# Optimization experiments

Hardware: AMD Instinct MI355X
Metric: run time of the kernel (lower is better)

## Reference

```python
import jax, jax.numpy as jnp
import numpy as np

N_NODES = 50000


def setup_inputs() -> dict:
    key = jax.random.key(0)
    k1, k2, k3, k4, k5, k6 = jax.random.split(key, 6)
    N, E, D, F = 50000, 800000, 512, 256
    feature_ori = jax.random.normal(k1, (N, D), dtype=jnp.float32)
    feature_aug = jax.random.normal(k2, (N, D), dtype=jnp.float32)
    edge_row = jax.random.randint(k3, (E,), 0, N, dtype=jnp.int32)
    edge_col = jax.random.randint(k4, (E,), 0, N, dtype=jnp.int32)
    edge_val = jax.random.uniform(k5, (E,), dtype=jnp.float32)
    # kaiming-uniform-ish init for weight, zeros for bias (as in reset_parameters)
    bound = float(np.sqrt(6.0 / D))
    weight = jax.random.uniform(k6, (D, F), dtype=jnp.float32, minval=-bound, maxval=bound)
    bias = jnp.zeros((F,), dtype=jnp.float32)
    return {
        "feature_ori": feature_ori,
        "feature_aug": feature_aug,
        "edge_row": edge_row,
        "edge_col": edge_col,
        "edge_val": edge_val,
        "weight": weight,
        "bias": bias,
    }


def _branch(feat, weight, bias, edge_row, edge_col, edge_val):
    # support = X @ W  -> [N, F]
    support = feat @ weight
    # sparse aggregation: out[i] = sum_{e: row[e]=i} val[e] * support[col[e]]
    msgs = edge_val[:, None] * support[edge_col]          # [E, F]
    out = jax.ops.segment_sum(msgs, edge_row, num_segments=N_NODES)
    return jax.nn.relu(out + bias)


def reference(feature_ori, feature_aug, edge_row, edge_col, edge_val, weight, bias):
    out_ori = _branch(feature_ori, weight, bias, edge_row, edge_col, edge_val)
    out_aug = _branch(feature_aug, weight, bias, edge_row, edge_col, edge_val)
    return (out_ori, out_aug)
```

## Files before the change

### kernel.cpp

```cpp
#include <hip/hip_runtime.h>
#include <hip/hip_bf16.h>

#define NNODES 50000
#define NEDGES 800000
#define DIN    512
#define FOUT   256

typedef __attribute__((ext_vector_type(8))) short short8;
typedef __attribute__((ext_vector_type(4))) float f32x4;
typedef __attribute__((ext_vector_type(4))) unsigned int u32x4;
typedef __attribute__((ext_vector_type(4))) unsigned short usv4;
typedef __attribute__((ext_vector_type(8))) unsigned short usv8;

static __device__ __forceinline__ unsigned short f2bf(float f) {
    unsigned int u = __float_as_uint(f);
    u += 0x7FFF + ((u >> 16) & 1);
    return (unsigned short)(u >> 16);
}
static __device__ __forceinline__ float bf2f(unsigned short h) {
    return __uint_as_float(((unsigned int)h) << 16);
}

__global__ void prep_kernel(const float* __restrict__ W, unsigned short* __restrict__ Wt,
                            const int* __restrict__ row, int* __restrict__ cnt) {
    int b = blockIdx.x;
    if (b < 512) {
        int o = b * 256 + threadIdx.x;
        int n = o >> 9, k = o & 511;
        Wt[o] = f2bf(W[k * FOUT + n]);
    } else {
        int e = (b - 512) * 256 + threadIdx.x;
        if (e < NEDGES) atomicAdd(&cnt[row[e]], 1);
    }
}

__global__ void scan_partial(const int* __restrict__ cnt, int* __restrict__ partial) {
    __shared__ int sm[256];
    int i = blockIdx.x * 256 + threadIdx.x;
    int v = (i < NNODES) ? cnt[i] : 0;
    sm[threadIdx.x] = v; __syncthreads();
    for (int s = 128; s > 0; s >>= 1) {
        if (threadIdx.x < s) sm[threadIdx.x] += sm[threadIdx.x + s];
        __syncthreads();
    }
    if (threadIdx.x == 0) partial[blockIdx.x] = sm[0];
}

__global__ void scan_exclusive_small(int* __restrict__ partial, int nb) {
    __shared__ int sm[256];
    int t = threadIdx.x;
    int v = (t < nb) ? partial[t] : 0;
    sm[t] = v; __syncthreads();
    for (int off = 1; off < 256; off <<= 1) {
        int add = (t >= off) ? sm[t - off] : 0;
        __syncthreads();
        sm[t] += add;
        __syncthreads();
    }
    if (t < nb) partial[t] = sm[t] - v;
}

__global__ void scan_write(const int* __restrict__ cnt, const int* __restrict__ partial,
                           int* __restrict__ row_start, int* __restrict__ cursor) {
    __shared__ int sm[256];
    int t = threadIdx.x;
    int i = blockIdx.x * 256 + t;
    int v = (i < NNODES) ? cnt[i] : 0;
    sm[t] = v; __syncthreads();
    for (int off = 1; off < 256; off <<= 1) {
        int add = (t >= off) ? sm[t - off] : 0;
        __syncthreads();
        sm[t] += add;
        __syncthreads();
    }
    if (i < NNODES) {
        int rs = partial[blockIdx.x] + sm[t] - v;
        row_start[i] = rs;
        cursor[i] = rs;
    }
    if (i == 0) row_start[NNODES] = NEDGES;
}

__global__ void scatter_kernel(const int* __restrict__ row, const int* __restrict__ col,
                               const float* __restrict__ val,
                               int* __restrict__ cursor, unsigned int* __restrict__ cv) {
    int e = blockIdx.x * 256 + threadIdx.x;
    if (e < NEDGES) {
        int r = row[e];
        int pos = atomicAdd(&cursor[r], 1);
        unsigned int vb = f2bf(val[e]);
        cv[pos] = (vb << 16) | (unsigned int)col[e];
    }
}

__global__ __launch_bounds__(512, 2)
void gemm_kernel(const float* __restrict__ Xo, const float* __restrict__ Xa,
                 const unsigned short* __restrict__ Wt,
                 unsigned short* __restrict__ S) {
    __shared__ __align__(16) unsigned short As[2][128][40];
    __shared__ __align__(16) unsigned short Bs[2][256][40];
    const int tid = threadIdx.x;
    const int branch = blockIdx.z;
    const float* __restrict__ X = branch ? Xa : Xo;
    const int boff = branch * 256;
    const int m_base = blockIdx.x * 128;
    const int lane = tid & 63, wave = tid >> 6;
    const int wm = (wave >> 2) * 64, wn = (wave & 3) * 64;
    const int quad = lane >> 4, r16 = lane & 15;

    f32x4 acc[4][4] = {};

    const int colf  = (tid & 7) * 4;
    const int rbase = tid >> 3;
    const int kseg  = (tid & 3) * 8;
    const int nrow  = tid >> 2;

    const int gm0 = m_base + rbase;
    const int gm1 = m_base + 64 + rbase;
    const bool va0 = gm0 < NNODES, va1 = gm1 < NNODES;
    const float* pA0 = &X[(long)gm0 * DIN + colf];
    const float* pA1 = &X[(long)gm1 * DIN + colf];
    const unsigned short* pB0 = &Wt[(long)nrow * DIN + kseg];
    const unsigned short* pB1 = &Wt[(long)(128 + nrow) * DIN + kseg];

    f32x4 fa0, fa1; u32x4 ub0, ub1;

#define GEMM_LOAD(K0)                                                          \
    do {                                                                       \
        fa0 = va0 ? __builtin_nontemporal_load((const f32x4*)(pA0 + (K0)))     \
                  : (f32x4)0.f;                                                \
        fa1 = va1 ? __builtin_nontemporal_load((const f32x4*)(pA1 + (K0)))     \
                  : (f32x4)0.f;                                                \
        ub0 = *(const u32x4*)(pB0 + (K0));                                     \
        ub1 = *(const u32x4*)(pB1 + (K0));                                     \
    } while (0)

#define GEMM_WRITE(B)                                                          \
    do {                                                                       \
        usv4 h0; h0.x = f2bf(fa0[0]); h0.y = f2bf(fa0[1]);                     \
        h0.z = f2bf(fa0[2]); h0.w = f2bf(fa0[3]);                              \
        *(usv4*)&As[B][rbase][colf] = h0;                                      \
        usv4 h1; h1.x = f2bf(fa1[0]); h1.y = f2bf(fa1[1]);                     \
        h1.z = f2bf(fa1[2]); h1.w = f2bf(fa1[3]);                              \
        *(usv4*)&As[B][64 + rbase][colf] = h1;                                 \
        *(u32x4*)&Bs[B][nrow][kseg] = ub0;                                     \
        *(u32x4*)&Bs[B][128 + nrow][kseg] = ub1;                               \
    } while (0)

#define GEMM_COMPUTE(B)                                                        \
    do {                                                                       \
        short8 a_frag[4], b_frag[4];                                           \
        _Pragma("unroll")                                                      \
        for (int mi = 0; mi < 4; mi++)                                         \
            a_frag[mi] = *(const short8*)&As[B][wm + mi * 16 + r16][quad * 8]; \
        _Pragma("unroll")                                                      \
        for (int ni = 0; ni < 4; ni++)                                         \
            b_frag[ni] = *(const short8*)&Bs[B][wn + ni * 16 + r16][quad * 8]; \
        _Pragma("unroll")                                                      \
        for (int mi = 0; mi < 4; mi++)                                         \
            _Pragma("unroll")                                                  \
            for (int ni = 0; ni < 4; ni++)                                     \
                acc[mi][ni] = __builtin_amdgcn_mfma_f32_16x16x32_bf16(         \
                    a_frag[mi], b_frag[ni], acc[mi][ni], 0, 0, 0);             \
    } while (0)

    GEMM_LOAD(0);
    GEMM_WRITE(0);
    __syncthreads();

    for (int k0 = 0; k0 < DIN; k0 += 64) {
        GEMM_LOAD(k0 + 32);
        GEMM_COMPUTE(0);
        GEMM_WRITE(1);
        __syncthreads();
        if (k0 + 64 < DIN) GEMM_LOAD(k0 + 64);
        GEMM_COMPUTE(1);
        if (k0 + 64 < DIN) GEMM_WRITE(0);
        __syncthreads();
    }

#undef GEMM_LOAD
#undef GEMM_WRITE
#undef GEMM_COMPUTE

    #pragma unroll
    for (int mi = 0; mi < 4; mi++) {
        #pragma unroll
        for (int rr = 0; rr < 4; rr++) {
            int m = m_base + wm + mi * 16 + quad * 4 + rr;
            if (m < NNODES) {
                #pragma unroll
                for (int ni = 0; ni < 4; ni++) {
                    int n = wn + ni * 16 + r16;
                    S[(long)m * 512 + boff + n] = f2bf(acc[mi][ni][rr]);
                }
            }
        }
    }
}

__global__ __launch_bounds__(256)
void aggregate_kernel(const int* __restrict__ row_start,
                      const unsigned int* __restrict__ cv,
                      const unsigned short* __restrict__ S,
                      const float* __restrict__ bias, float* __restrict__ out) {
    int node = blockIdx.x * 4 + (threadIdx.x >> 6);
    int lane = threadIdx.x & 63;
    if (node >= NNODES) return;
    int s = row_start[node], e = row_start[node + 1];
    const int f8 = (lane & 31) * 8;
    const long soff = (long)(lane >> 5) * 256 + f8;
    float a0 = 0.f, a1 = 0.f, a2 = 0.f, a3 = 0.f;
    float a4 = 0.f, a5 = 0.f, a6 = 0.f, a7 = 0.f;

#define LOADG(C0, C1, C2, C3, Q0, Q1, Q2, Q3, I)                               \
    do {                                                                       \
        C0 = __builtin_nontemporal_load(&cv[(I)]);                             \
        C1 = __builtin_nontemporal_load(&cv[(I) + 1]);                         \
        C2 = __builtin_nontemporal_load(&cv[(I) + 2]);                         \
        C3 = __builtin_nontemporal_load(&cv[(I) + 3]);                         \
        Q0 = *(const usv8*)&S[(long)(C0 & 0xFFFFu) * 512 + soff];              \
        Q1 = *(const usv8*)&S[(long)(C1 & 0xFFFFu) * 512 + soff];              \
        Q2 = *(const usv8*)&S[(long)(C2 & 0xFFFFu) * 512 + soff];              \
        Q3 = *(const usv8*)&S[(long)(C3 & 0xFFFFu) * 512 + soff];              \
    } while (0)

#define EDGE_FMA(Cw, Q)                                                        \
    do {                                                                       \
        float v = bf2f((unsigned short)((Cw) >> 16));                          \
        a0 = fmaf(v, bf2f((Q)[0]), a0); a1 = fmaf(v, bf2f((Q)[1]), a1);        \
        a2 = fmaf(v, bf2f((Q)[2]), a2); a3 = fmaf(v, bf2f((Q)[3]), a3);        \
        a4 = fmaf(v, bf2f((Q)[4]), a4); a5 = fmaf(v, bf2f((Q)[5]), a5);        \
        a6 = fmaf(v, bf2f((Q)[6]), a6); a7 = fmaf(v, bf2f((Q)[7]), a7);        \
    } while (0)

#define FMAG(C0, C1, C2, C3, Q0, Q1, Q2, Q3)                                   \
    do {                                                                       \
        EDGE_FMA(C0, Q0); EDGE_FMA(C1, Q1);                                    \
        EDGE_FMA(C2, Q2); EDGE_FMA(C3, Q3);                                    \
    } while (0)

    unsigned int c0, c1, c2, c3, d0, d1, d2, d3;
    usv8 qa0, qa1, qa2, qa3, qb0, qb1, qb2, qb3;

    int idx = s;
    int r = (e - s) >> 2;
    if (r > 0) {
        LOADG(c0, c1, c2, c3, qa0, qa1, qa2, qa3, idx); idx += 4; r--;
        while (r >= 2) {
            LOADG(d0, d1, d2, d3, qb0, qb1, qb2, qb3, idx); idx += 4;
            FMAG(c0, c1, c2, c3, qa0, qa1, qa2, qa3);
            LOADG(c0, c1, c2, c3, qa0, qa1, qa2, qa3, idx); idx += 4;
            FMAG(d0, d1, d2, d3, qb0, qb1, qb2, qb3);
            r -= 2;
        }
        if (r == 1) {
            LOADG(d0, d1, d2, d3, qb0, qb1, qb2, qb3, idx); idx += 4;
            FMAG(c0, c1, c2, c3, qa0, qa1, qa2, qa3);
            FMAG(d0, d1, d2, d3, qb0, qb1, qb2, qb3);
        } else {
            FMAG(c0, c1, c2, c3, qa0, qa1, qa2, qa3);
        }
    }
    for (; idx < e; idx++) {
        unsigned int w = __builtin_nontemporal_load(&cv[idx]);
        usv8 q = *(const usv8*)&S[(long)(w & 0xFFFFu) * 512 + soff];
        EDGE_FMA(w, q);
    }

#undef LOADG
#undef EDGE_FMA
#undef FMAG

    f32x4 b0 = *(const f32x4*)&bias[f8];
    f32x4 b1 = *(const f32x4*)&bias[f8 + 4];
    long o = (long)(lane >> 5) * NNODES * FOUT + (long)node * FOUT + f8;
    f32x4 r0, r1;
    r0[0] = fmaxf(a0 + b0[0], 0.f); r0[1] = fmaxf(a1 + b0[1], 0.f);
    r0[2] = fmaxf(a2 + b0[2], 0.f); r0[3] = fmaxf(a3 + b0[3], 0.f);
    r1[0] = fmaxf(a4 + b1[0], 0.f); r1[1] = fmaxf(a5 + b1[1], 0.f);
    r1[2] = fmaxf(a6 + b1[2], 0.f); r1[3] = fmaxf(a7 + b1[3], 0.f);
    __builtin_nontemporal_store(r0, (f32x4*)&out[o]);
    __builtin_nontemporal_store(r1, (f32x4*)&out[o + 4]);
}

extern "C" void kernel_launch(void* const* d_in, const int* in_sizes, int n_in,
                              void* d_out, int out_size, void* d_ws, size_t ws_size,
                              hipStream_t stream) {
    const float* Xo   = (const float*)d_in[0];
    const float* Xa   = (const float*)d_in[1];
    const int*   erow = (const int*)d_in[2];
    const int*   ecol = (const int*)d_in[3];
    const float* eval_= (const float*)d_in[4];
    const float* W    = (const float*)d_in[5];
    const float* bias = (const float*)d_in[6];
    float* out = (float*)d_out;

    char* ws = (char*)d_ws;
    unsigned short* S         = (unsigned short*)(ws);
    unsigned short* Wt        = (unsigned short*)(ws + 51200000);
    int*            cnt       = (int*)(ws + 51462144);
    int*            row_start = (int*)(ws + 51662144);
    int*            partial   = (int*)(ws + 51862208);
    unsigned int*   cv        = (unsigned int*)(ws + 51863232);

    (void)in_sizes; (void)n_in; (void)out_size; (void)ws_size;

    hipMemsetAsync(cnt, 0, 200000, stream);
    prep_kernel<<<3637, 256, 0, stream>>>(W, Wt, erow, cnt);
    scan_partial<<<196, 256, 0, stream>>>(cnt, partial);
    scan_exclusive_small<<<1, 256, 0, stream>>>(partial, 196);
    scan_write<<<196, 256, 0, stream>>>(cnt, partial, row_start, cnt);
    scatter_kernel<<<3125, 256, 0, stream>>>(erow, ecol, eval_, cnt, cv);

    dim3 gg(391, 1, 2);
    gemm_kernel<<<gg, 512, 0, stream>>>(Xo, Xa, Wt, S);

    aggregate_kernel<<<12500, 256, 0, stream>>>(row_start, cv, S, bias, out);
}
```

Before: 487.0 us.

## Split aggregation into per-branch passes with half-wave edge parallelism

Aggregation now runs as two launches, one per branch (ori/aug). Within each pass the two half-waves take alternate edges of the same node, then combine partial sums with a cross-lane shuffle before writing. The aim is to shrink the working set of gathered S rows per pass so it fits better in cache and improves gather locality. In exchange it adds a second launch, reads the edge list twice, and adds shuffle-reduction overhead.

```diff
diff --git a/kernel.cpp b/kernel.cpp
--- a/kernel.cpp
+++ b/kernel.cpp
@@ -200,88 +200,113 @@
 }
 
 __global__ __launch_bounds__(256)
-void aggregate_kernel(const int* __restrict__ row_start,
-                      const unsigned int* __restrict__ cv,
-                      const unsigned short* __restrict__ S,
-                      const float* __restrict__ bias, float* __restrict__ out) {
-    int node = blockIdx.x * 4 + (threadIdx.x >> 6);
-    int lane = threadIdx.x & 63;
+void aggregate_pass(const int* __restrict__ row_start,
+                    const unsigned int* __restrict__ cv,
+                    const unsigned short* __restrict__ S,
+                    const float* __restrict__ bias, float* __restrict__ out,
+                    const int half) {
+    const int node = __builtin_amdgcn_readfirstlane(blockIdx.x * 4 + (threadIdx.x >> 6));
     if (node >= NNODES) return;
-    int s = row_start[node], e = row_start[node + 1];
-    const int f8 = (lane & 31) * 8;
-    const long soff = (long)(lane >> 5) * 256 + f8;
+    const int lane = threadIdx.x & 63;
+    const int fl = (lane & 31) * 8;
+    const unsigned int sub = lane >> 5;
+    const long soff = (long)half * 256 + fl;
+    const int s = row_start[node], e = row_start[node + 1];
+
     float a0 = 0.f, a1 = 0.f, a2 = 0.f, a3 = 0.f;
     float a4 = 0.f, a5 = 0.f, a6 = 0.f, a7 = 0.f;
 
-#define LOADG(C0, C1, C2, C3, Q0, Q1, Q2, Q3, I)                               \
-    do {                                                                       \
-        C0 = __builtin_nontemporal_load(&cv[(I)]);                             \
-        C1 = __builtin_nontemporal_load(&cv[(I) + 1]);                         \
-        C2 = __builtin_nontemporal_load(&cv[(I) + 2]);                         \
-        C3 = __builtin_nontemporal_load(&cv[(I) + 3]);                         \
-        Q0 = *(const usv8*)&S[(long)(C0 & 0xFFFFu) * 512 + soff];              \
-        Q1 = *(const usv8*)&S[(long)(C1 & 0xFFFFu) * 512 + soff];              \
-        Q2 = *(const usv8*)&S[(long)(C2 & 0xFFFFu) * 512 + soff];              \
-        Q3 = *(const usv8*)&S[(long)(C3 & 0xFFFFu) * 512 + soff];              \
-    } while (0)
-
-#define EDGE_FMA(Cw, Q)                                                        \
-    do {                                                                       \
-        float v = bf2f((unsigned short)((Cw) >> 16));                          \
+#define PLOAD(CW0, CW1, Q)                                                     \
+    do {                                                                       \
+        unsigned int cw_ = sub ? (CW1) : (CW0);                                \
+        Q = *(const usv8*)&S[(long)(cw_ & 0xFFFFu) * 512 + soff];              \
+    } while (0)
+
+#define PFMA(CW0, CW1, Q)                                                      \
+    do {                                                                       \
+        unsigned int cw_ = sub ? (CW1) : (CW0);                                \
+        float v = bf2f((unsigned short)(cw_ >> 16));                           \
         a0 = fmaf(v, bf2f((Q)[0]), a0); a1 = fmaf(v, bf2f((Q)[1]), a1);        \
         a2 = fmaf(v, bf2f((Q)[2]), a2); a3 = fmaf(v, bf2f((Q)[3]), a3);        \
         a4 = fmaf(v, bf2f((Q)[4]), a4); a5 = fmaf(v, bf2f((Q)[5]), a5);        \
         a6 = fmaf(v, bf2f((Q)[6]), a6); a7 = fmaf(v, bf2f((Q)[7]), a7);        \
     } while (0)
 
-#define FMAG(C0, C1, C2, C3, Q0, Q1, Q2, Q3)                                   \
-    do {                                                                       \
-        EDGE_FMA(C0, Q0); EDGE_FMA(C1, Q1);                                    \
-        EDGE_FMA(C2, Q2); EDGE_FMA(C3, Q3);                                    \
-    } while (0)
-
-    unsigned int c0, c1, c2, c3, d0, d1, d2, d3;
+#define LOADG(C0, C1, C2, C3, C4, C5, C6, C7, Q0, Q1, Q2, Q3, I)               \
+    do {                                                                       \
+        C0 = cv[(I)];     C1 = cv[(I) + 1]; C2 = cv[(I) + 2]; C3 = cv[(I) + 3];\
+        C4 = cv[(I) + 4]; C5 = cv[(I) + 5]; C6 = cv[(I) + 6]; C7 = cv[(I) + 7];\
+        PLOAD(C0, C1, Q0); PLOAD(C2, C3, Q1);                                  \
+        PLOAD(C4, C5, Q2); PLOAD(C6, C7, Q3);                                  \
+    } while (0)
+
+#define FMAG(C0, C1, C2, C3, C4, C5, C6, C7, Q0, Q1, Q2, Q3)                   \
+    do {                                                                       \
+        PFMA(C0, C1, Q0); PFMA(C2, C3, Q1);                                    \
+        PFMA(C4, C5, Q2); PFMA(C6, C7, Q3);                                    \
+    } while (0)
+
+    unsigned int c0, c1, c2, c3, c4, c5, c6, c7;
+    unsigned int d0, d1, d2, d3, d4, d5, d6, d7;
     usv8 qa0, qa1, qa2, qa3, qb0, qb1, qb2, qb3;
 
     int idx = s;
-    int r = (e - s) >> 2;
+    int r = (e - s) >> 3;
     if (r > 0) {
-        LOADG(c0, c1, c2, c3, qa0, qa1, qa2, qa3, idx); idx += 4; r--;
+        LOADG(c0, c1, c2, c3, c4, c5, c6, c7, qa0, qa1, qa2, qa3, idx); idx += 8; r--;
         while (r >= 2) {
-            LOADG(d0, d1, d2, d3, qb0, qb1, qb2, qb3, idx); idx += 4;
-            FMAG(c0, c1, c2, c3, qa0, qa1, qa2, qa3);
-            LOADG(c0, c1, c2, c3, qa0, qa1, qa2, qa3, idx); idx += 4;
-            FMAG(d0, d1, d2, d3, qb0, qb1, qb2, qb3);
+            LOADG(d0, d1, d2, d3, d4, d5, d6, d7, qb0, qb1, qb2, qb3, idx); idx += 8;
+            FMAG(c0, c1, c2, c3, c4, c5, c6, c7, qa0, qa1, qa2, qa3);
+            LOADG(c0, c1, c2, c3, c4, c5, c6, c7, qa0, qa1, qa2, qa3, idx); idx += 8;
+            FMAG(d0, d1, d2, d3, d4, d5, d6, d7, qb0, qb1, qb2, qb3);
             r -= 2;
         }
         if (r == 1) {
-            LOADG(d0, d1, d2, d3, qb0, qb1, qb2, qb3, idx); idx += 4;
-            FMAG(c0, c1, c2, c3, qa0, qa1, qa2, qa3);
-            FMAG(d0, d1, d2, d3, qb0, qb1, qb2, qb3);
+            LOADG(d0, d1, d2, d3, d4, d5, d6, d7, qb0, qb1, qb2, qb3, idx); idx += 8;
+            FMAG(c0, c1, c2, c3, c4, c5, c6, c7, qa0, qa1, qa2, qa3);
+            FMAG(d0, d1, d2, d3, d4, d5, d6, d7, qb0, qb1, qb2, qb3);
         } else {
-            FMAG(c0, c1, c2, c3, qa0, qa1, qa2, qa3);
+            FMAG(c0, c1, c2, c3, c4, c5, c6, c7, qa0, qa1, qa2, qa3);
         }
     }
-    for (; idx < e; idx++) {
-        unsigned int w = __builtin_nontemporal_load(&cv[idx]);
+    for (; idx + 2 <= e; idx += 2) {
+        unsigned int w0 = cv[idx], w1 = cv[idx + 1];
+        usv8 q;
+        PLOAD(w0, w1, q);
+        PFMA(w0, w1, q);
+    }
+    if (idx < e) {
+        unsigned int w = cv[idx];
         usv8 q = *(const usv8*)&S[(long)(w & 0xFFFFu) * 512 + soff];
-        EDGE_FMA(w, q);
-    }
-
+        float v = sub ? 0.f : bf2f((unsigned short)(w >> 16));
+        a0 = fmaf(v, bf2f(q[0]), a0); a1 = fmaf(v, bf2f(q[1]), a1);
+        a2 = fmaf(v, bf2f(q[2]), a2); a3 = fmaf(v, bf2f(q[3]), a3);
+        a4 = fmaf(v, bf2f(q[4]), a4); a5 = fmaf(v, bf2f(q[5]), a5);
+        a6 = fmaf(v, bf2f(q[6]), a6); a7 = fmaf(v, bf2f(q[7]), a7);
+    }
+
+#undef PLOAD
+#undef PFMA
 #undef LOADG
-#undef EDGE_FMA
 #undef FMAG
 
-    f32x4 b0 = *(const f32x4*)&bias[f8];
-    f32x4 b1 = *(const f32x4*)&bias[f8 + 4];
-    long o = (long)(lane >> 5) * NNODES * FOUT + (long)node * FOUT + f8;
-    f32x4 r0, r1;
-    r0[0] = fmaxf(a0 + b0[0], 0.f); r0[1] = fmaxf(a1 + b0[1], 0.f);
-    r0[2] = fmaxf(a2 + b0[2], 0.f); r0[3] = fmaxf(a3 + b0[3], 0.f);
-    r1[0] = fmaxf(a4 + b1[0], 0.f); r1[1] = fmaxf(a5 + b1[1], 0.f);
-    r1[2] = fmaxf(a6 + b1[2], 0.f); r1[3] = fmaxf(a7 + b1[3], 0.f);
-    __builtin_nontemporal_store(r0, (f32x4*)&out[o]);
-    __builtin_nontemporal_store(r1, (f32x4*)&out[o + 4]);
+    a0 += __shfl_xor(a0, 32); a1 += __shfl_xor(a1, 32);
+    a2 += __shfl_xor(a2, 32); a3 += __shfl_xor(a3, 32);
+    a4 += __shfl_xor(a4, 32); a5 += __shfl_xor(a5, 32);
+    a6 += __shfl_xor(a6, 32); a7 += __shfl_xor(a7, 32);
+
+    if (lane < 32) {
+        f32x4 b0 = *(const f32x4*)&bias[fl];
+        f32x4 b1 = *(const f32x4*)&bias[fl + 4];
+        long o = (long)half * NNODES * FOUT + (long)node * FOUT + fl;
+        f32x4 r0, r1;
+        r0[0] = fmaxf(a0 + b0[0], 0.f); r0[1] = fmaxf(a1 + b0[1], 0.f);
+        r0[2] = fmaxf(a2 + b0[2], 0.f); r0[3] = fmaxf(a3 + b0[3], 0.f);
+        r1[0] = fmaxf(a4 + b1[0], 0.f); r1[1] = fmaxf(a5 + b1[1], 0.f);
+        r1[2] = fmaxf(a6 + b1[2], 0.f); r1[3] = fmaxf(a7 + b1[3], 0.f);
+        __builtin_nontemporal_store(r0, (f32x4*)&out[o]);
+        __builtin_nontemporal_store(r1, (f32x4*)&out[o + 4]);
+    }
 }
 
 extern "C" void kernel_launch(void* const* d_in, const int* in_sizes, int n_in,
@@ -316,5 +341,6 @@
     dim3 gg(391, 1, 2);
     gemm_kernel<<<gg, 512, 0, stream>>>(Xo, Xa, Wt, S);
 
-    aggregate_kernel<<<12500, 256, 0, stream>>>(row_start, cv, S, bias, out);
-}
+    aggregate_pass<<<12500, 256, 0, stream>>>(row_start, cv, S, bias, out, 0);
+    aggregate_pass<<<12500, 256, 0, stream>>>(row_start, cv, S, bias, out, 1);
+}
```

Measured after the change: 482.5 us. About the same (-0.9%).
